# Kernel optimization log

Measured on AMD Instinct MI355X. Metric: run time of the kernel, lower is better.

Reference implementation:

```python
import jax, jax.numpy as jnp
import numpy as np

B, S, E, D = 4, 2048, 1024, 1024
NEG_INF = float('-inf')


def setup_inputs() -> dict:
    key = jax.random.key(0)
    ks = jax.random.split(key, 10)
    query = jax.random.normal(ks[0], (B, S, E), dtype=jnp.float32)
    key_t = jax.random.normal(ks[1], (B, S, E), dtype=jnp.float32)
    value = jax.random.normal(ks[2], (B, S, E), dtype=jnp.float32)
    # Linear params (torch convention: y = x @ W.T + b)
    sc = 1.0 / np.sqrt(E)
    Wq = jax.random.uniform(ks[3], (D, E), jnp.float32, -sc, sc)
    bq = jax.random.uniform(ks[4], (D,), jnp.float32, -sc, sc)
    Wk = jax.random.uniform(ks[5], (D, E), jnp.float32, -sc, sc)
    bk = jax.random.uniform(ks[6], (D,), jnp.float32, -sc, sc)
    Wv = jax.random.uniform(ks[7], (D, E), jnp.float32, -sc, sc)
    bv = jax.random.uniform(ks[8], (D,), jnp.float32, -sc, sc)
    # padding mask: True = masked key position; ensure key 0 is never masked
    # so no row is fully -inf under the causal mask.
    lengths = jax.random.randint(ks[9], (B, 1, 1), 1, S + 1)  # valid length per batch
    pos = jnp.arange(S)[None, None, :]
    padding_mask = pos >= lengths  # [B,1,S] bool
    return {
        "query": query, "key": key_t, "value": value,
        "Wq": Wq, "bq": bq, "Wk": Wk, "bk": bk, "Wv": Wv, "bv": bv,
        "padding_mask": padding_mask, "look_ahead_mask": 1,
    }


def reference(query, key, value, Wq, bq, Wk, bk, Wv, bv, padding_mask, look_ahead_mask):
    q = query @ Wq.T + bq          # [B,S,D]
    k = key @ Wk.T + bk            # [B,S,D]
    v = value @ Wv.T + bv          # [B,S,D]
    scale = jnp.sqrt(jnp.asarray(q.shape[-1], q.dtype))
    qk = jnp.einsum('bqd,bkd->bqk', q, k) / scale  # [B,S,S]
    if padding_mask is not None:
        qk = jnp.where(padding_mask, NEG_INF, qk)
    if look_ahead_mask:
        causal = jnp.where(
            jnp.tril(jnp.ones((q.shape[1], k.shape[1]), dtype=bool)),
            jnp.asarray(0.0, qk.dtype), jnp.asarray(NEG_INF, qk.dtype))
        qk = qk + causal
    attn = jax.nn.softmax(qk, axis=-1)
    return jnp.einsum('bqk,bkd->bqd', attn, v)  # [B,S,D]
```

## Files before the change

kernel.cpp:

```cpp
#include <hip/hip_runtime.h>
#include <cstdint>
#include <cstddef>

#define B_ 4
#define S_ 2048
#define E_ 1024
#define D_ 1024
#define MFLAT (B_*S_)

typedef __attribute__((ext_vector_type(4))) float f32x4;
typedef __attribute__((ext_vector_type(8))) short short8;
typedef unsigned short u16;
typedef unsigned int   u32;

__device__ __forceinline__ u16 f2bf(float f) {
  u32 u = __float_as_uint(f);
  u = (u + 0x7fffu + ((u >> 16) & 1u)) >> 16;
  return (u16)u;
}

__device__ __forceinline__ void gll16(const void* g, void* lds) {
  __builtin_amdgcn_global_load_lds(
      (const __attribute__((address_space(1))) void*)g,
      (__attribute__((address_space(3))) void*)lds, 16, 0, 0);
}

#define BARRIER() do { asm volatile("" ::: "memory"); \
                       __builtin_amdgcn_s_barrier();  \
                       asm volatile("" ::: "memory"); } while (0)

__device__ __forceinline__ void gemm256_core(
    const u16* __restrict__ Ag, int lda,
    const u16* __restrict__ Bg, int ldb,
    int NT, char* lds, f32x4 acc[8][4])
{
  const int tid = threadIdx.x;
  const int w  = tid >> 6;
  const int l  = tid & 63;
  const int wm = w >> 2;
  const int wn = w & 3;

  const int srow = tid >> 3;
  const int scs  = ((tid & 7) << 4) ^ ((srow & 7) << 4);

  const int fr = l & 15;
  const int kq = l >> 4;
  const int kcol0 = (kq << 4) ^ ((l & 7) << 4);
  const int kcol1 = ((kq << 4) + 64) ^ ((l & 7) << 4);
  const int aoff = wm * 16384 + fr * 128;
  const int boff = 65536 + (wn >> 1) * 16384 + (((wn & 1) * 64 + fr) * 128);

  const int nhalf = 4 * NT;

#define STAGE_HALF(h_) do {                                                        \
    const int h__ = (h_);                                                          \
    if (h__ < nhalf) {                                                             \
      const int T__ = h__ >> 2, r__ = h__ & 3, buf__ = T__ & 1;                    \
      const char* s0; char* d0; size_t rstep;                                      \
      if (r__ < 2) {                                                               \
        s0 = (const char*)Bg + ((((size_t)(r__*128 + srow)) * (size_t)ldb          \
                                 + (size_t)T__*64) << 1) + scs;                    \
        d0 = lds + 65536 + buf__*32768 + r__*16384 + (w << 10);                    \
        rstep = ((size_t)ldb) << 7;                                                \
      } else {                                                                     \
        s0 = (const char*)Ag + ((((size_t)((r__-2)*128 + srow)) * (size_t)lda      \
                                 + (size_t)T__*64) << 1) + scs;                    \
        d0 = lds + buf__*32768 + (r__-2)*16384 + (w << 10);                        \
        rstep = ((size_t)lda) << 7;                                                \
      }                                                                            \
      gll16(s0, d0);                                                               \
      gll16(s0 + rstep, d0 + 8192);                                                \
    }                                                                              \
  } while (0)

#define LDA_F(mf, kc) (*(const short8*)(lds + bufo + aoff + (mf)*2048 + (kc)))
#define LDB_F(nf, kc) (*(const short8*)(lds + bufo + boff + (nf)*2048 + (kc)))

#define WAIT_LGKM() do { asm volatile("s_waitcnt lgkmcnt(0)" ::: "memory"); \
                         __builtin_amdgcn_sched_barrier(0); } while (0)

#define MFMA_Q(jbase) do {                                                         \
    __builtin_amdgcn_s_setprio(1);                                                 \
    _Pragma("unroll")                                                              \
    for (int i = 0; i < 4; ++i) {                                                  \
      _Pragma("unroll")                                                            \
      for (int j = 0; j < 2; ++j) {                                                \
        acc[accm + i][(jbase) + j] = __builtin_amdgcn_mfma_f32_16x16x32_bf16(      \
            areg[i][0], breg[(jbase)+j][0], acc[accm + i][(jbase)+j], 0, 0, 0);    \
        acc[accm + i][(jbase) + j] = __builtin_amdgcn_mfma_f32_16x16x32_bf16(      \
            areg[i][1], breg[(jbase)+j][1], acc[accm + i][(jbase)+j], 0, 0, 0);    \
      }                                                                            \
    }                                                                              \
    __builtin_amdgcn_s_setprio(0);                                                 \
  } while (0)

  short8 areg[4][2], breg[4][2];

  STAGE_HALF(0); STAGE_HALF(1); STAGE_HALF(2); STAGE_HALF(3);
  STAGE_HALF(4); STAGE_HALF(5);
  asm volatile("s_waitcnt vmcnt(4)" ::: "memory");
  BARRIER();

  for (int t = 0; t < NT; ++t) {
    const int bufo = (t & 1) << 15;
    const int hb = 4 * t + 6;

    {
      int accm = 0;
#pragma unroll
      for (int i = 0; i < 4; ++i) { areg[i][0] = LDA_F(i, kcol0); areg[i][1] = LDA_F(i, kcol1); }
#pragma unroll
      for (int j = 0; j < 2; ++j) { breg[j][0] = LDB_F(j, kcol0); breg[j][1] = LDB_F(j, kcol1); }
      STAGE_HALF(hb + 0);
      BARRIER();
      WAIT_LGKM();
      MFMA_Q(0);
      BARRIER();
    }
    {
      int accm = 0;
#pragma unroll
      for (int j = 2; j < 4; ++j) { breg[j][0] = LDB_F(j, kcol0); breg[j][1] = LDB_F(j, kcol1); }
      STAGE_HALF(hb + 1);
      BARRIER();
      WAIT_LGKM();
      MFMA_Q(2);
      BARRIER();
    }
    {
      int accm = 4;
#pragma unroll
      for (int i = 0; i < 4; ++i) { areg[i][0] = LDA_F(4 + i, kcol0); areg[i][1] = LDA_F(4 + i, kcol1); }
      STAGE_HALF(hb + 2);
      BARRIER();
      WAIT_LGKM();
      MFMA_Q(0);
      BARRIER();
    }
    {
      int accm = 4;
      STAGE_HALF(hb + 3);
      BARRIER();
      WAIT_LGKM();
      MFMA_Q(2);
      asm volatile("s_waitcnt vmcnt(4)" ::: "memory");
      BARRIER();
    }
  }
#undef STAGE_HALF
#undef LDA_F
#undef LDB_F
#undef WAIT_LGKM
#undef MFMA_Q
}

__device__ __forceinline__ void gemm_core(
    const u16* __restrict__ Ag, int lda,
    const u16* __restrict__ Bg, int ldb,
    int ksteps, u16* As, u16* Bs, f32x4 acc[4][4])
{
  const int tid = threadIdx.x;
  const int w = tid >> 6;
  const int l = tid & 63;
  const int srow = l >> 2;
  const int skb  = (l & 3) << 3;
  const int fr = l & 15;
  const int fk = (l >> 4) << 3;
  const int wr = (w >> 1) << 6;
  const int wc = (w & 1) << 6;
  const int c0 = w * 2, c1 = c0 + 1;

  const u16* a0 = Ag + (size_t)(c0*16 + srow)*lda + skb;
  const u16* a1 = Ag + (size_t)(c1*16 + srow)*lda + skb;
  const u16* b0 = Bg + (size_t)(c0*16 + srow)*ldb + skb;
  const u16* b1 = Bg + (size_t)(c1*16 + srow)*ldb + skb;

  for (int kt = 0; kt < ksteps; ++kt) {
    gll16(a0, As + c0*512);
    gll16(a1, As + c1*512);
    gll16(b0, Bs + c0*512);
    gll16(b1, Bs + c1*512);
    a0 += 32; a1 += 32; b0 += 32; b1 += 32;
    __syncthreads();
    short8 af[4], bfr[4];
#pragma unroll
    for (int i = 0; i < 4; ++i)
      af[i] = *(const short8*)(As + ((wr + i*16 + fr) << 5) + fk);
#pragma unroll
    for (int j = 0; j < 4; ++j)
      bfr[j] = *(const short8*)(Bs + ((wc + j*16 + fr) << 5) + fk);
#pragma unroll
    for (int i = 0; i < 4; ++i)
#pragma unroll
      for (int j = 0; j < 4; ++j)
        acc[i][j] = __builtin_amdgcn_mfma_f32_16x16x32_bf16(af[i], bfr[j], acc[i][j], 0, 0, 0);
    __syncthreads();
  }
}

__global__ __launch_bounds__(256) void cvt_kernel(const float* __restrict__ src,
                                                  u16* __restrict__ dst, int n4) {
  int idx = blockIdx.x * blockDim.x + threadIdx.x;
  int stride = gridDim.x * blockDim.x;
  for (int i = idx; i < n4; i += stride) {
    float4 f = ((const float4*)src)[i];
    ushort4 o;
    o.x = f2bf(f.x); o.y = f2bf(f.y); o.z = f2bf(f.z); o.w = f2bf(f.w);
    ((ushort4*)dst)[i] = o;
  }
}

__global__ __launch_bounds__(256) void lengths_kernel(const void* __restrict__ mask,
                                                      int* __restrict__ lengths) {
  __shared__ int isbytes;
  const int t = threadIdx.x;
  if (t == 0) isbytes = 0;
  __syncthreads();
  const int* wi = (const int*)mask;
  int bad = 0;
  for (int idx = t; idx < (B_*S_)/4; idx += 256) {
    int v = wi[idx];
    if (v != 0 && v != 1) bad = 1;
  }
  if (bad) atomicOr(&isbytes, 1);
  __syncthreads();
  const int isb = isbytes;
  const int w = t >> 6, l = t & 63;
  const unsigned char* mb = (const unsigned char*)mask;
  int cnt = 0;
  for (int j = l; j < S_; j += 64) {
    int val = isb ? (int)mb[(size_t)w*S_ + j] : wi[(size_t)w*S_ + j];
    cnt += (val == 0);
  }
#pragma unroll
  for (int off = 32; off >= 1; off >>= 1) cnt += __shfl_xor(cnt, off);
  if (l == 0) lengths[w] = cnt;
}

__global__ __launch_bounds__(512, 2) void proj256_kernel(
    const u16* __restrict__ X, const u16* __restrict__ W,
    const float* __restrict__ bq, const float* __restrict__ bk, const float* __restrict__ bv,
    u16* __restrict__ q, u16* __restrict__ k, u16* __restrict__ v)
{
  extern __shared__ char lds[];
  const int nt = blockIdx.x, mt = blockIdx.y, z = blockIdx.z;
  const u16* Xz = X + (size_t)z * ((size_t)MFLAT * E_) + (size_t)(mt*256)*E_;
  const u16* Wz = W + (size_t)z * ((size_t)D_ * E_)    + (size_t)(nt*256)*E_;
  f32x4 acc[8][4];
#pragma unroll
  for (int i = 0; i < 8; ++i)
#pragma unroll
    for (int j = 0; j < 4; ++j) acc[i][j] = (f32x4){0.f,0.f,0.f,0.f};

  gemm256_core(Xz, E_, Wz, E_, E_/64, lds, acc);

  const float* bias = (z == 0) ? bq : (z == 1) ? bk : bv;
  u16* out = (z == 0) ? q : (z == 1) ? k : v;
  const int tid = threadIdx.x, w = tid >> 6, l = tid & 63;
  const int wm = w >> 2, wn = w & 3;
  const int fr = l & 15, kq = l >> 4;
  const int orow0 = mt*256 + wm*128 + kq*4;
  const int ocol0 = nt*256 + wn*64 + fr;
#pragma unroll
  for (int nf = 0; nf < 4; ++nf) {
    const int col = ocol0 + nf*16;
    const float bcol = bias[col];
#pragma unroll
    for (int mf = 0; mf < 8; ++mf)
#pragma unroll
      for (int r = 0; r < 4; ++r)
        out[(size_t)(orow0 + mf*16 + r)*D_ + col] = f2bf(acc[mf][nf][r] + bcol);
  }
}

__global__ __launch_bounds__(256) void transpose_kernel(
    const u16* __restrict__ v, u16* __restrict__ vT)
{
  __shared__ u16 tl[64][68];
  const int xt = blockIdx.x;
  const int yt = blockIdx.y;
  const int b  = blockIdx.z;
  const int t = threadIdx.x;
  const int r0 = t >> 4;
  const int c4 = (t & 15) << 2;
  const u16* src = v + ((size_t)b*S_ + yt*64)*D_ + xt*64;
#pragma unroll
  for (int rr = r0; rr < 64; rr += 16) {
    ushort4 u = *(const ushort4*)(src + (size_t)rr*D_ + c4);
    tl[rr][c4+0] = u.x; tl[rr][c4+1] = u.y; tl[rr][c4+2] = u.z; tl[rr][c4+3] = u.w;
  }
  __syncthreads();
  u16* dst = vT + ((size_t)b*D_ + xt*64)*S_ + yt*64;
#pragma unroll
  for (int rr = r0; rr < 64; rr += 16) {
    ushort4 u;
    u.x = tl[c4+0][rr]; u.y = tl[c4+1][rr]; u.z = tl[c4+2][rr]; u.w = tl[c4+3][rr];
    *(ushort4*)(dst + (size_t)rr*S_ + c4) = u;
  }
}

__global__ __launch_bounds__(512, 2) void qk256_kernel(
    const u16* __restrict__ q, const u16* __restrict__ k,
    const int* __restrict__ lengths, float* __restrict__ scores)
{
  const int tx = blockIdx.x, ty = blockIdx.y, b = blockIdx.z;
  if (tx > ty) return;
  const int len = lengths[b];
  if (tx * 256 >= len) return;
  extern __shared__ char lds[];
  f32x4 acc[8][4];
#pragma unroll
  for (int i = 0; i < 8; ++i)
#pragma unroll
    for (int j = 0; j < 4; ++j) acc[i][j] = (f32x4){0.f,0.f,0.f,0.f};
  const u16* Aq = q + ((size_t)b*S_ + (size_t)ty*256) * D_;
  const u16* Bk = k + ((size_t)b*S_ + (size_t)tx*256) * D_;
  gemm256_core(Aq, D_, Bk, D_, D_/64, lds, acc);

  const int tid = threadIdx.x, w = tid >> 6, l = tid & 63;
  const int wm = w >> 2, wn = w & 3;
  const int fr = l & 15, kq = l >> 4;
  const int orow0 = ty*256 + wm*128 + kq*4;
  const int ocol0 = tx*256 + wn*64 + fr;
  float* sb = scores + (size_t)b*S_*S_;
#pragma unroll
  for (int mf = 0; mf < 8; ++mf)
#pragma unroll
    for (int nf = 0; nf < 4; ++nf)
#pragma unroll
      for (int r = 0; r < 4; ++r)
        sb[(size_t)(orow0 + mf*16 + r)*S_ + (ocol0 + nf*16)] = acc[mf][nf][r] * 0.03125f;
}

__global__ __launch_bounds__(256) void softmax_kernel(
    const float* __restrict__ scores, const int* __restrict__ lengths,
    u16* __restrict__ P)
{
  const int i = blockIdx.x, b = blockIdx.y;
  const int len = lengths[b];
  const int kmax = min(i + 1, len);
  const float* row = scores + ((size_t)b*S_ + i)*S_;
  u16* prow = P + ((size_t)b*S_ + i)*S_;
  const int t = threadIdx.x;
  const int j0 = t * 8;
  float v[8];
  {
    float4 x0 = *(const float4*)(row + j0);
    float4 x1 = *(const float4*)(row + j0 + 4);
    v[0]=x0.x; v[1]=x0.y; v[2]=x0.z; v[3]=x0.w;
    v[4]=x1.x; v[5]=x1.y; v[6]=x1.z; v[7]=x1.w;
  }
  float m = -3.4e38f;
#pragma unroll
  for (int e = 0; e < 8; ++e) if (j0 + e < kmax) m = fmaxf(m, v[e]);
#pragma unroll
  for (int off = 32; off >= 1; off >>= 1) m = fmaxf(m, __shfl_xor(m, off));
  __shared__ float redm[4], reds[4];
  if ((t & 63) == 0) redm[t >> 6] = m;
  __syncthreads();
  m = fmaxf(fmaxf(redm[0], redm[1]), fmaxf(redm[2], redm[3]));
  float s = 0.f, ex[8];
#pragma unroll
  for (int e = 0; e < 8; ++e) {
    ex[e] = (j0 + e < kmax) ? __expf(v[e] - m) : 0.f;
    s += ex[e];
  }
#pragma unroll
  for (int off = 32; off >= 1; off >>= 1) s += __shfl_xor(s, off);
  if ((t & 63) == 0) reds[t >> 6] = s;
  __syncthreads();
  s = reds[0] + reds[1] + reds[2] + reds[3];
  const float inv = 1.0f / s;
  short8 o;
#pragma unroll
  for (int e = 0; e < 8; ++e) o[e] = (short)f2bf(ex[e] * inv);
  *(short8*)(prow + j0) = o;
}

__global__ __launch_bounds__(256) void pv_kernel(
    const u16* __restrict__ P, const u16* __restrict__ vT,
    const int* __restrict__ lengths, float* __restrict__ out)
{
  const int xt = blockIdx.x, ty = blockIdx.y, b = blockIdx.z;
  const int len = lengths[b];
  const int kend = min(ty*128 + 128, len);
  const int ksteps = (kend + 31) >> 5;
  __shared__ u16 As[4096], Bs[4096];
  f32x4 acc[4][4];
#pragma unroll
  for (int i = 0; i < 4; ++i)
#pragma unroll
    for (int j = 0; j < 4; ++j) acc[i][j] = (f32x4){0.f,0.f,0.f,0.f};
  const u16* Ap = P  + ((size_t)b*S_ + (size_t)ty*128)*S_;
  const u16* Bv = vT + ((size_t)b*D_ + (size_t)xt*128)*S_;
  gemm_core(Ap, S_, Bv, S_, ksteps, As, Bs, acc);

  const int tid = threadIdx.x, w = tid >> 6, l = tid & 63;
  const int wr = (w >> 1) << 6, wc = (w & 1) << 6;
  const int orow = ty*128 + wr + ((l >> 4) << 2);
  const int ocol = xt*128 + wc + (l & 15);
  float* ob = out + (size_t)b*S_*D_;
#pragma unroll
  for (int i = 0; i < 4; ++i)
#pragma unroll
    for (int j = 0; j < 4; ++j)
#pragma unroll
      for (int r = 0; r < 4; ++r)
        ob[(size_t)(orow + i*16 + r)*D_ + (ocol + j*16)] = acc[i][j][r];
}

extern "C" void kernel_launch(void* const* d_in, const int* in_sizes, int n_in,
                              void* d_out, int out_size, void* d_ws, size_t ws_size,
                              hipStream_t stream)
{
  const float* query = (const float*)d_in[0];
  const float* key_  = (const float*)d_in[1];
  const float* value = (const float*)d_in[2];
  const float* Wq = (const float*)d_in[3];
  const float* bq = (const float*)d_in[4];
  const float* Wk = (const float*)d_in[5];
  const float* bk = (const float*)d_in[6];
  const float* Wv = (const float*)d_in[7];
  const float* bv = (const float*)d_in[8];
  const void*  pmask = d_in[9];
  float* out = (float*)d_out;
  char* ws = (char*)d_ws;

  (void)hipFuncSetAttribute((const void*)proj256_kernel,
                            hipFuncAttributeMaxDynamicSharedMemorySize, 131072);
  (void)hipFuncSetAttribute((const void*)qk256_kernel,
                            hipFuncAttributeMaxDynamicSharedMemorySize, 131072);

  int* lengths = (int*)ws;
  u16* q   = (u16*)(ws + 256);
  u16* kk  = q  + (size_t)MFLAT * D_;
  u16* vT  = kk + (size_t)MFLAT * D_;
  u16* Pbuf = (u16*)(ws + 50331904ull);
  u16* vbuf = Pbuf;
  char* scratch = ws + 83886336ull;
  u16* Xb = (u16*)scratch;
  u16* Wb = Xb + 3ull * MFLAT * E_;
  float* scores = (float*)scratch;

  cvt_kernel<<<dim3(2048), 256, 0, stream>>>(query, Xb,                 (MFLAT*E_)/4);
  cvt_kernel<<<dim3(2048), 256, 0, stream>>>(key_,  Xb + (size_t)MFLAT*E_,   (MFLAT*E_)/4);
  cvt_kernel<<<dim3(2048), 256, 0, stream>>>(value, Xb + 2ull*MFLAT*E_, (MFLAT*E_)/4);
  cvt_kernel<<<dim3(256),  256, 0, stream>>>(Wq, Wb,                    (D_*E_)/4);
  cvt_kernel<<<dim3(256),  256, 0, stream>>>(Wk, Wb + (size_t)D_*E_,    (D_*E_)/4);
  cvt_kernel<<<dim3(256),  256, 0, stream>>>(Wv, Wb + 2ull*D_*E_,       (D_*E_)/4);
  lengths_kernel<<<dim3(1), 256, 0, stream>>>(pmask, lengths);

  proj256_kernel<<<dim3(4, 32, 3), 512, 131072, stream>>>(Xb, Wb, bq, bk, bv, q, kk, vbuf);

  transpose_kernel<<<dim3(16, 32, 4), 256, 0, stream>>>(vbuf, vT);

  qk256_kernel<<<dim3(8, 8, 4), 512, 131072, stream>>>(q, kk, lengths, scores);

  softmax_kernel<<<dim3(2048, 4), 256, 0, stream>>>(scores, lengths, Pbuf);

  pv_kernel<<<dim3(8, 16, 4), 256, 0, stream>>>(Pbuf, vT, lengths, out);
}
```

Before: 373.2 us.

## Remap GEMM grids for XCD-aware locality, compact causal tiles, merge convert launches

The projection and QK GEMMs move to 1D grids with an XCD-aware block remap, so that consecutive tiles sharing operands land on the same XCD's L2. The QK kernel now launches only the lower-triangular tiles and decodes them with an sqrt-based index, removing the early-exit blocks. The six fp32-to-bf16 conversion launches become two, and the sched_barrier after the LDS wait is dropped so the compiler can schedule more freely. The per-element segment division in the converter and the relaxed scheduling could add overhead.

```diff
diff --git a/kernel.cpp b/kernel.cpp
--- a/kernel.cpp
+++ b/kernel.cpp
@@ -76,8 +76,7 @@
 #define LDA_F(mf, kc) (*(const short8*)(lds + bufo + aoff + (mf)*2048 + (kc)))
 #define LDB_F(nf, kc) (*(const short8*)(lds + bufo + boff + (nf)*2048 + (kc)))
 
-#define WAIT_LGKM() do { asm volatile("s_waitcnt lgkmcnt(0)" ::: "memory"); \
-                         __builtin_amdgcn_sched_barrier(0); } while (0)
+#define WAIT_LGKM() asm volatile("s_waitcnt lgkmcnt(0)" ::: "memory")
 
 #define MFMA_Q(jbase) do {                                                         \
     __builtin_amdgcn_s_setprio(1);                                                 \
@@ -198,12 +197,18 @@
   }
 }
 
-__global__ __launch_bounds__(256) void cvt_kernel(const float* __restrict__ src,
-                                                  u16* __restrict__ dst, int n4) {
+__global__ __launch_bounds__(256) void cvt3_kernel(
+    const float* __restrict__ s0, const float* __restrict__ s1,
+    const float* __restrict__ s2, u16* __restrict__ dst, int segn4)
+{
   int idx = blockIdx.x * blockDim.x + threadIdx.x;
   int stride = gridDim.x * blockDim.x;
-  for (int i = idx; i < n4; i += stride) {
-    float4 f = ((const float4*)src)[i];
+  const int total = 3 * segn4;
+  for (int i = idx; i < total; i += stride) {
+    int s = i / segn4;
+    int off = i - s * segn4;
+    const float4* sp = (s == 0) ? (const float4*)s0 : (s == 1) ? (const float4*)s1 : (const float4*)s2;
+    float4 f = sp[off];
     ushort4 o;
     o.x = f2bf(f.x); o.y = f2bf(f.y); o.z = f2bf(f.z); o.w = f2bf(f.w);
     ((ushort4*)dst)[i] = o;
@@ -243,7 +248,13 @@
     u16* __restrict__ q, u16* __restrict__ k, u16* __restrict__ v)
 {
   extern __shared__ char lds[];
-  const int nt = blockIdx.x, mt = blockIdx.y, z = blockIdx.z;
+  const int bid = blockIdx.x;
+  const int wg = (bid & 7) * 48 + (bid >> 3);
+  const int z  = wg >> 7;
+  const int rem = wg & 127;
+  const int nt = rem >> 5;
+  const int mt = rem & 31;
+
   const u16* Xz = X + (size_t)z * ((size_t)MFLAT * E_) + (size_t)(mt*256)*E_;
   const u16* Wz = W + (size_t)z * ((size_t)D_ * E_)    + (size_t)(nt*256)*E_;
   f32x4 acc[8][4];
@@ -303,8 +314,15 @@
     const u16* __restrict__ q, const u16* __restrict__ k,
     const int* __restrict__ lengths, float* __restrict__ scores)
 {
-  const int tx = blockIdx.x, ty = blockIdx.y, b = blockIdx.z;
-  if (tx > ty) return;
+  const int bid = blockIdx.x;
+  const int wg = (bid & 7) * 18 + (bid >> 3);
+  const int b = wg / 36;
+  const int r = wg - b * 36;
+  int ty = (int)((sqrtf(8.0f * (float)r + 1.0f) - 1.0f) * 0.5f);
+  while ((ty + 1) * (ty + 2) / 2 <= r) ++ty;
+  while (ty * (ty + 1) / 2 > r) --ty;
+  const int tx = r - ty * (ty + 1) / 2;
+
   const int len = lengths[b];
   if (tx * 256 >= len) return;
   extern __shared__ char lds[];
@@ -328,8 +346,8 @@
 #pragma unroll
     for (int nf = 0; nf < 4; ++nf)
 #pragma unroll
-      for (int r = 0; r < 4; ++r)
-        sb[(size_t)(orow0 + mf*16 + r)*S_ + (ocol0 + nf*16)] = acc[mf][nf][r] * 0.03125f;
+      for (int r2 = 0; r2 < 4; ++r2)
+        sb[(size_t)(orow0 + mf*16 + r2)*S_ + (ocol0 + nf*16)] = acc[mf][nf][r2] * 0.03125f;
 }
 
 __global__ __launch_bounds__(256) void softmax_kernel(
@@ -442,19 +460,15 @@
   u16* Wb = Xb + 3ull * MFLAT * E_;
   float* scores = (float*)scratch;
 
-  cvt_kernel<<<dim3(2048), 256, 0, stream>>>(query, Xb,                 (MFLAT*E_)/4);
-  cvt_kernel<<<dim3(2048), 256, 0, stream>>>(key_,  Xb + (size_t)MFLAT*E_,   (MFLAT*E_)/4);
-  cvt_kernel<<<dim3(2048), 256, 0, stream>>>(value, Xb + 2ull*MFLAT*E_, (MFLAT*E_)/4);
-  cvt_kernel<<<dim3(256),  256, 0, stream>>>(Wq, Wb,                    (D_*E_)/4);
-  cvt_kernel<<<dim3(256),  256, 0, stream>>>(Wk, Wb + (size_t)D_*E_,    (D_*E_)/4);
-  cvt_kernel<<<dim3(256),  256, 0, stream>>>(Wv, Wb + 2ull*D_*E_,       (D_*E_)/4);
+  cvt3_kernel<<<dim3(2048), 256, 0, stream>>>(query, key_, value, Xb, (MFLAT*E_)/4);
+  cvt3_kernel<<<dim3(512),  256, 0, stream>>>(Wq, Wk, Wv, Wb, (D_*E_)/4);
   lengths_kernel<<<dim3(1), 256, 0, stream>>>(pmask, lengths);
 
-  proj256_kernel<<<dim3(4, 32, 3), 512, 131072, stream>>>(Xb, Wb, bq, bk, bv, q, kk, vbuf);
+  proj256_kernel<<<dim3(384), 512, 131072, stream>>>(Xb, Wb, bq, bk, bv, q, kk, vbuf);
 
   transpose_kernel<<<dim3(16, 32, 4), 256, 0, stream>>>(vbuf, vT);
 
-  qk256_kernel<<<dim3(8, 8, 4), 512, 131072, stream>>>(q, kk, lengths, scores);
+  qk256_kernel<<<dim3(144), 512, 131072, stream>>>(q, kk, lengths, scores);
 
   softmax_kernel<<<dim3(2048, 4), 256, 0, stream>>>(scores, lengths, Pbuf);
 
```

New measurement: 355.1 us. 1.05x faster.
